# Performance work log

Hardware: AMD Instinct MI355X
Metric: run time of the kernel (lower is better)

The kernel has to match this reference:

```python
import jax, jax.numpy as jnp
import numpy as np

B, T, H, E, D, K = 4, 4096, 2048, 8, 1024, 2

def setup_inputs() -> dict:
    key = jax.random.key(0)
    ks = jax.random.split(key, 7)
    x  = jax.random.normal(ks[0], (B, T, H), dtype=jnp.float32)
    Wr = jax.random.normal(ks[1], (H, E), dtype=jnp.float32) * (1.0 / np.sqrt(H))
    br = jnp.zeros((E,), dtype=jnp.float32)
    We = jax.random.normal(ks[2], (E, H, D), dtype=jnp.float32) * (1.0 / np.sqrt(H))
    be = jnp.zeros((E, D), dtype=jnp.float32)
    Wc = jax.random.normal(ks[3], (D, H), dtype=jnp.float32) * (1.0 / np.sqrt(D))
    bc = jnp.zeros((H,), dtype=jnp.float32)
    return {"x": x, "Wr": Wr, "br": br, "We": We, "be": be, "Wc": Wc, "bc": bc}

def reference(x, Wr, br, We, be, Wc, bc):
    # Router: [B,T,H] @ [H,E] -> [B,T,E]
    router_logits = jnp.einsum('bth,he->bte', x, Wr) + br
    scores = jax.nn.softmax(router_logits, axis=-1)
    # top-k over experts (sorted descending, like torch.topk)
    topk_scores, topk_idx = jax.lax.top_k(scores, K)  # [B,T,K]
    # Dense all-expert linear: [B,T,E,D]
    expert_outs = jnp.einsum('bth,ehd->bted', x, We) + be
    # Gather the chosen experts per token: [B,T,K,D]
    gather_idx = jnp.broadcast_to(topk_idx[..., None], (B, T, K, D))
    chosen = jnp.take_along_axis(expert_outs, gather_idx, axis=2)
    # Weighted sum over top-k: [B,T,D]
    weighted = jnp.sum(chosen * topk_scores[..., None], axis=2)
    # Combine: [B,T,D] @ [D,H] -> [B,T,H]
    return jnp.einsum('btd,dh->bth', weighted, Wc) + bc
```

## Files before the change

kernel.cpp:

```cpp
#include <hip/hip_runtime.h>
#include <hip/hip_bf16.h>

typedef float f32x4 __attribute__((ext_vector_type(4)));
typedef short bf16x8 __attribute__((ext_vector_type(8)));

#define M_NT 16
#define M_OFF 17
#define M_TBL 32
#define MAX_TILES 264
#define NCHUNK 1024

__device__ __forceinline__ void gload16(const void* g, void* l) {
  __builtin_amdgcn_global_load_lds(
      (const __attribute__((address_space(1))) void*)g,
      (__attribute__((address_space(3))) void*)l, 16, 0, 0);
}

__device__ __forceinline__ float bf2f(unsigned short u) {
  union { unsigned int i; float f; } v; v.i = ((unsigned int)u) << 16; return v.f;
}
__device__ __forceinline__ unsigned short f2bf(float f) {
  __hip_bfloat16 h = __float2bfloat16(f);
  return __builtin_bit_cast(unsigned short, h);
}

#define CBAR() do { asm volatile("" ::: "memory"); __builtin_amdgcn_s_barrier(); asm volatile("" ::: "memory"); } while (0)
#define VMC4() asm volatile("s_waitcnt vmcnt(4)" ::: "memory")
#define VMC0() asm volatile("s_waitcnt vmcnt(0)" ::: "memory")

__global__ void transpose_cvt(const float* __restrict__ src,
                              unsigned short* __restrict__ dst, int R, int C) {
  __shared__ float tile[32][33];
  int b = blockIdx.z;
  int c0 = blockIdx.x * 32, r0 = blockIdx.y * 32;
  src += (size_t)b * R * C;
  dst += (size_t)b * R * C;
  int tx = threadIdx.x, ty = threadIdx.y;
#pragma unroll
  for (int i = 0; i < 32; i += 8)
    tile[ty + i][tx] = src[(size_t)(r0 + ty + i) * C + c0 + tx];
  __syncthreads();
#pragma unroll
  for (int i = 0; i < 32; i += 8)
    dst[(size_t)(c0 + ty + i) * R + r0 + tx] = f2bf(tile[tx][ty + i]);
}

__global__ __launch_bounds__(256) void router_kernel(
    const float* __restrict__ x, const float* __restrict__ Wr,
    const float* __restrict__ br, unsigned short* __restrict__ xbf,
    float* __restrict__ scores, int* __restrict__ idx,
    int* __restrict__ blk_hist) {
  __shared__ int cnt[8];
  int tid = threadIdx.x, lane = tid & 63, w = tid >> 6;
  if (tid < 8) cnt[tid] = 0;
  __syncthreads();
  int t0 = blockIdx.x * 16 + w * 4;
  const float* xr = x + (size_t)t0 * 2048;
  unsigned short* xo = xbf + (size_t)t0 * 2048;
  float acc[4][8] = {};
#pragma unroll
  for (int j = 0; j < 8; ++j) {
    int h0 = j * 256 + lane * 4;
    float4 xv[4];
#pragma unroll
    for (int t = 0; t < 4; ++t) xv[t] = *(const float4*)(xr + (size_t)t * 2048 + h0);
#pragma unroll
    for (int t = 0; t < 4; ++t) {
      ushort4 p;
      p.x = f2bf(xv[t].x); p.y = f2bf(xv[t].y);
      p.z = f2bf(xv[t].z); p.w = f2bf(xv[t].w);
      *(ushort4*)(xo + (size_t)t * 2048 + h0) = p;
    }
    const float4* wp = (const float4*)(Wr + (size_t)h0 * 8);
#pragma unroll
    for (int c = 0; c < 4; ++c) {
      float4 w0 = wp[2 * c], w1 = wp[2 * c + 1];
      float xc0 = (c == 0) ? xv[0].x : (c == 1) ? xv[0].y : (c == 2) ? xv[0].z : xv[0].w;
      float xc1 = (c == 0) ? xv[1].x : (c == 1) ? xv[1].y : (c == 2) ? xv[1].z : xv[1].w;
      float xc2 = (c == 0) ? xv[2].x : (c == 1) ? xv[2].y : (c == 2) ? xv[2].z : xv[2].w;
      float xc3 = (c == 0) ? xv[3].x : (c == 1) ? xv[3].y : (c == 2) ? xv[3].z : xv[3].w;
      acc[0][0] += xc0 * w0.x; acc[0][1] += xc0 * w0.y; acc[0][2] += xc0 * w0.z; acc[0][3] += xc0 * w0.w;
      acc[0][4] += xc0 * w1.x; acc[0][5] += xc0 * w1.y; acc[0][6] += xc0 * w1.z; acc[0][7] += xc0 * w1.w;
      acc[1][0] += xc1 * w0.x; acc[1][1] += xc1 * w0.y; acc[1][2] += xc1 * w0.z; acc[1][3] += xc1 * w0.w;
      acc[1][4] += xc1 * w1.x; acc[1][5] += xc1 * w1.y; acc[1][6] += xc1 * w1.z; acc[1][7] += xc1 * w1.w;
      acc[2][0] += xc2 * w0.x; acc[2][1] += xc2 * w0.y; acc[2][2] += xc2 * w0.z; acc[2][3] += xc2 * w0.w;
      acc[2][4] += xc2 * w1.x; acc[2][5] += xc2 * w1.y; acc[2][6] += xc2 * w1.z; acc[2][7] += xc2 * w1.w;
      acc[3][0] += xc3 * w0.x; acc[3][1] += xc3 * w0.y; acc[3][2] += xc3 * w0.z; acc[3][3] += xc3 * w0.w;
      acc[3][4] += xc3 * w1.x; acc[3][5] += xc3 * w1.y; acc[3][6] += xc3 * w1.z; acc[3][7] += xc3 * w1.w;
    }
  }
#pragma unroll
  for (int t = 0; t < 4; ++t)
#pragma unroll
    for (int e = 0; e < 8; ++e)
#pragma unroll
      for (int off = 32; off > 0; off >>= 1)
        acc[t][e] += __shfl_xor(acc[t][e], off);
  if (lane < 4) {
    int t = t0 + lane;
    float l[8];
#pragma unroll
    for (int e = 0; e < 8; ++e) {
      float v = (lane == 0) ? acc[0][e] : (lane == 1) ? acc[1][e]
              : (lane == 2) ? acc[2][e] : acc[3][e];
      l[e] = v + br[e];
    }
    float mx = l[0];
#pragma unroll
    for (int e = 1; e < 8; ++e) mx = fmaxf(mx, l[e]);
    float se = 0.f;
#pragma unroll
    for (int e = 0; e < 8; ++e) se += __expf(l[e] - mx);
    float inv = 1.f / se;
    int e1 = 0; float b1 = l[0];
#pragma unroll
    for (int e = 1; e < 8; ++e) if (l[e] > b1) { b1 = l[e]; e1 = e; }
    int e2 = -1; float b2 = -1e30f;
#pragma unroll
    for (int e = 0; e < 8; ++e) if (e != e1 && l[e] > b2) { b2 = l[e]; e2 = e; }
    idx[2 * t] = e1; idx[2 * t + 1] = e2;
    scores[2 * t] = __expf(b1 - mx) * inv;
    scores[2 * t + 1] = __expf(b2 - mx) * inv;
    atomicAdd(&cnt[e1], 1);
    atomicAdd(&cnt[e2], 1);
  }
  __syncthreads();
  if (tid < 8) blk_hist[blockIdx.x * 8 + tid] = cnt[tid];
}

__global__ __launch_bounds__(512) void scan_kernel(
    const int* __restrict__ blk_hist, int* __restrict__ chunk_base,
    int* __restrict__ meta, int* __restrict__ rowlist) {
  __shared__ int stot[8], soff[8];
  int tid = threadIdx.x, lane = tid & 63, e = tid >> 6;
  int running = 0;
  for (int g = 0; g < NCHUNK / 64; ++g) {
    int c = g * 64 + lane;
    int v = blk_hist[c * 8 + e];
    int orig = v;
#pragma unroll
    for (int off = 1; off < 64; off <<= 1) {
      int n = __shfl_up(v, off);
      if (lane >= off) v += n;
    }
    chunk_base[c * 8 + e] = running + v - orig;
    running += __shfl(v, 63);
  }
  if (lane == 0) stot[e] = running;
  __syncthreads();
  if (tid == 0) {
    int off = 0, nt = 0;
    int4* tbl = (int4*)(meta + M_TBL);
    for (int ee = 0; ee < 8; ++ee) {
      int c = stot[ee];
      meta[M_OFF + ee] = off; soff[ee] = off;
      int tiles = (c + 127) >> 7;
      for (int t = 0; t < tiles; ++t)
        tbl[nt++] = make_int4(ee, off + t * 128, min(128, c - t * 128), 0);
      off += tiles << 7;
    }
    meta[M_NT] = nt;
  }
  __syncthreads();
  for (int ee = 0; ee < 8; ++ee) {
    int c = stot[ee], end = ((c + 127) >> 7) << 7;
    for (int i = c + tid; i < end; i += 512) rowlist[soff[ee] + i] = 0;
  }
}

__global__ void scatter_kernel(const int* __restrict__ idx,
                               const int* __restrict__ chunk_base,
                               const int* __restrict__ meta,
                               int* __restrict__ rowlist) {
  int c = blockIdx.x, lane = threadIdx.x;
  int entry = c * 32 + lane;
  int e = (lane < 32) ? idx[entry] : -1;
#pragma unroll
  for (int ee = 0; ee < 8; ++ee) {
    unsigned long long m = __ballot(e == ee);
    if (e == ee) {
      int rank = __popcll(m & ((1ull << lane) - 1));
      rowlist[meta[M_OFF + ee] + chunk_base[c * 8 + ee] + rank] = entry;
    }
  }
}


#define RD_FRAGS(BUFB) do { \
  _Pragma("unroll") for (int m_ = 0; m_ < 4; ++m_) \
    av[m_] = *(const bf16x8*)(aP + (BUFB) + m_ * 1024); \
  _Pragma("unroll") for (int n_ = 0; n_ < 4; ++n_) \
    bv[n_] = *(const bf16x8*)(bP + (BUFB) + n_ * 1024); \
} while (0)

#define MFMA16() do { \
  __builtin_amdgcn_s_setprio(1); \
  _Pragma("unroll") for (int m_ = 0; m_ < 4; ++m_) \
  _Pragma("unroll") for (int n_ = 0; n_ < 4; ++n_) \
    acc[m_][n_] = __builtin_amdgcn_mfma_f32_16x16x32_bf16(av[m_], bv[n_], acc[m_][n_], 0, 0, 0); \
  __builtin_amdgcn_s_setprio(0); \
} while (0)

#define STAGE(BUFB, KOFF) do { \
  gload16(pA0 + (KOFF), dA + (BUFB)); \
  gload16(pA1 + (KOFF), dA + (BUFB) + 4096); \
  gload16(pB0 + (KOFF), dB + (BUFB)); \
  gload16(pB1 + (KOFF), dB + (BUFB) + 4096); \
} while (0)

__global__ __launch_bounds__(256, 4) void expert_gemm(
    const unsigned short* __restrict__ xbf,
    const unsigned short* __restrict__ WeT,
    const float* __restrict__ be,
    const float* __restrict__ scores,
    const int* __restrict__ rowlist,
    const int* __restrict__ meta,
    unsigned short* __restrict__ z) {
  __shared__ char smem[32768];
  __shared__ int lrows[128];
  int nt = meta[M_NT];
  int flat = blockIdx.y * 8 + blockIdx.x;
  int work = (flat & 7) * MAX_TILES + (flat >> 3);
  int tileid = work >> 3, nb = work & 7;
  if (tileid >= nt) return;
  int4 tt = ((const int4*)(meta + M_TBL))[tileid];
  int e = tt.x, base = tt.y, valid = tt.z;
  int n0 = nb * 128;
  int tid = threadIdx.x, lane = tid & 63, w = tid >> 6;
  if (tid < 128) lrows[tid] = rowlist[base + tid];
  __syncthreads();
  int wm = w >> 1, wn = w & 1;
  int fl = lane & 15, q = lane >> 4;
  int rA = tid >> 2;
  int sl = ((tid & 3) ^ ((rA >> 1) & 3)) * 16;
  const char* pA0 = (const char*)xbf + (size_t)(lrows[rA] >> 1) * 4096 + sl;
  const char* pA1 = (const char*)xbf + (size_t)(lrows[rA + 64] >> 1) * 4096 + sl;
  const char* pB0 = (const char*)WeT + ((size_t)e * 1024 + n0 + rA) * 4096 + sl;
  const char* pB1 = (const char*)WeT + ((size_t)e * 1024 + n0 + rA + 64) * 4096 + sl;
  char* dA = smem + tid * 16;
  char* dB = smem + 8192 + tid * 16;
  int swz = ((fl >> 1) & 3) << 4;
  const char* aP = smem + (wm * 64 + fl) * 64 + ((q * 16) ^ swz);
  const char* bP = smem + 8192 + (wn * 64 + fl) * 64 + ((q * 16) ^ swz);
  STAGE(0, 0); STAGE(16384, 64);
  VMC4(); CBAR();
  f32x4 acc[4][4] = {};
  bf16x8 av[4], bv[4];
  const int NT = 64;
  for (int t2 = 0; t2 < NT; t2 += 2) {
    int koff = t2 * 64;
    RD_FRAGS(0);
    MFMA16();
    CBAR();
    if (t2 + 2 < NT) { STAGE(0, koff + 128); VMC4(); } else { VMC0(); }
    CBAR();
    RD_FRAGS(16384);
    MFMA16();
    CBAR();
    if (t2 + 3 < NT) { STAGE(16384, koff + 192); VMC4(); } else { VMC0(); }
    CBAR();
  }
  float bev[4];
#pragma unroll
  for (int nc = 0; nc < 4; ++nc)
    bev[nc] = be[e * 1024 + n0 + wn * 64 + nc * 16 + fl];
#pragma unroll
  for (int mi = 0; mi < 4; ++mi) {
    int rowbase = wm * 64 + mi * 16 + q * 4;
#pragma unroll
    for (int r = 0; r < 4; ++r) {
      int row = rowbase + r;
      if (row < valid) {
        int entry = lrows[row];
        float s = scores[entry];
        unsigned short* zr = z + (size_t)entry * 1024 + n0 + wn * 64 + fl;
#pragma unroll
        for (int nc = 0; nc < 4; ++nc)
          zr[nc * 16] = f2bf((acc[mi][nc][r] + bev[nc]) * s);
      }
    }
  }
}

__global__ __launch_bounds__(256, 4) void combine_gemm(
    const unsigned short* __restrict__ y,
    const unsigned short* __restrict__ WcT,
    const float* __restrict__ bc,
    float* __restrict__ out) {
  __shared__ char smem[32768];
  int flat = blockIdx.y * 8 + blockIdx.x;
  int work = (flat & 7) * 256 + (flat >> 3);
  int mt = work >> 4, nb = work & 15;
  int m0 = mt * 128, n0 = nb * 128;
  int tid = threadIdx.x, lane = tid & 63, w = tid >> 6;
  int wm = w >> 1, wn = w & 1;
  int fl = lane & 15, q = lane >> 4;
  int rA = tid >> 2;
  int sl = ((tid & 3) ^ ((rA >> 1) & 3)) * 16;
  const char* pA0 = (const char*)y + (size_t)(m0 + rA) * 2048 + sl;
  const char* pA1 = (const char*)y + (size_t)(m0 + rA + 64) * 2048 + sl;
  const char* pB0 = (const char*)WcT + (size_t)(n0 + rA) * 2048 + sl;
  const char* pB1 = (const char*)WcT + (size_t)(n0 + rA + 64) * 2048 + sl;
  char* dA = smem + tid * 16;
  char* dB = smem + 8192 + tid * 16;
  int swz = ((fl >> 1) & 3) << 4;
  const char* aP = smem + (wm * 64 + fl) * 64 + ((q * 16) ^ swz);
  const char* bP = smem + 8192 + (wn * 64 + fl) * 64 + ((q * 16) ^ swz);
  STAGE(0, 0); STAGE(16384, 64);
  VMC4(); CBAR();
  f32x4 acc[4][4] = {};
  bf16x8 av[4], bv[4];
  const int NT = 32;
  for (int t2 = 0; t2 < NT; t2 += 2) {
    int koff = t2 * 64;
    RD_FRAGS(0);
    MFMA16();
    CBAR();
    if (t2 + 2 < NT) { STAGE(0, koff + 128); VMC4(); } else { VMC0(); }
    CBAR();
    RD_FRAGS(16384);
    MFMA16();
    CBAR();
    if (t2 + 3 < NT) { STAGE(16384, koff + 192); VMC4(); } else { VMC0(); }
    CBAR();
  }
  float bcv[4];
#pragma unroll
  for (int nc = 0; nc < 4; ++nc)
    bcv[nc] = bc[n0 + wn * 64 + nc * 16 + fl];
#pragma unroll
  for (int mi = 0; mi < 4; ++mi) {
    int rowbase = m0 + wm * 64 + mi * 16 + q * 4;
#pragma unroll
    for (int r = 0; r < 4; ++r) {
      float* orow = out + (size_t)(rowbase + r) * 2048 + n0 + wn * 64 + fl;
#pragma unroll
      for (int nc = 0; nc < 4; ++nc)
        orow[nc * 16] = acc[mi][nc][r] + bcv[nc];
    }
  }
}

__global__ void wsum_kernel(const unsigned short* __restrict__ z,
                            unsigned short* __restrict__ y) {
  size_t i = ((size_t)blockIdx.x * 256 + threadIdx.x) * 8;
  size_t t = i >> 10, d = i & 1023;
  int4 za = *(const int4*)(z + (t * 2) * 1024 + d);
  int4 zb = *(const int4*)(z + (t * 2 + 1) * 1024 + d);
  int4 r;
  const unsigned short* pa = (const unsigned short*)&za;
  const unsigned short* pb = (const unsigned short*)&zb;
  unsigned short* pr = (unsigned short*)&r;
#pragma unroll
  for (int j = 0; j < 8; ++j) pr[j] = f2bf(bf2f(pa[j]) + bf2f(pb[j]));
  *(int4*)(y + i) = r;
}

extern "C" void kernel_launch(void* const* d_in, const int* in_sizes, int n_in,
                              void* d_out, int out_size, void* d_ws, size_t ws_size,
                              hipStream_t stream) {
  const float* x  = (const float*)d_in[0];
  const float* Wr = (const float*)d_in[1];
  const float* br = (const float*)d_in[2];
  const float* We = (const float*)d_in[3];
  const float* be = (const float*)d_in[4];
  const float* Wc = (const float*)d_in[5];
  const float* bc = (const float*)d_in[6];
  float* out = (float*)d_out;

  char* ws = (char*)d_ws;
  size_t o = 0;
  auto alloc = [&](size_t b) {
    char* p = ws + o;
    o = (o + b + 255) & ~(size_t)255;
    return p;
  };
  unsigned short* xbf = (unsigned short*)alloc(16384UL * 2048 * 2);
  unsigned short* WeT = (unsigned short*)alloc(8UL * 1024 * 2048 * 2);
  unsigned short* WcT = (unsigned short*)alloc(2048UL * 1024 * 2);
  unsigned short* z   = (unsigned short*)alloc(32768UL * 1024 * 2);
  unsigned short* yw  = (unsigned short*)alloc(16384UL * 1024 * 2);
  float* scores = (float*)alloc(32768UL * 4);
  int* idx      = (int*)alloc(32768UL * 4);
  int* rowlist  = (int*)alloc(36864UL * 4);
  int* meta     = (int*)alloc(8192);
  int* blk_hist = (int*)alloc(NCHUNK * 8 * 4);
  int* chunk_base = (int*)alloc(NCHUNK * 8 * 4);
  (void)ws_size; (void)in_sizes; (void)n_in; (void)out_size;

  hipLaunchKernelGGL(transpose_cvt, dim3(32, 64, 8), dim3(32, 8), 0, stream, We, WeT, 2048, 1024);
  hipLaunchKernelGGL(transpose_cvt, dim3(64, 32, 1), dim3(32, 8), 0, stream, Wc, WcT, 1024, 2048);
  hipLaunchKernelGGL(router_kernel, dim3(NCHUNK), dim3(256), 0, stream, x, Wr, br, xbf, scores, idx, blk_hist);
  hipLaunchKernelGGL(scan_kernel, dim3(1), dim3(512), 0, stream, blk_hist, chunk_base, meta, rowlist);
  hipLaunchKernelGGL(scatter_kernel, dim3(NCHUNK), dim3(64), 0, stream, idx, chunk_base, meta, rowlist);
  hipLaunchKernelGGL(expert_gemm, dim3(8, MAX_TILES), dim3(256), 0, stream,
                     xbf, WeT, be, scores, rowlist, meta, z);
  hipLaunchKernelGGL(wsum_kernel, dim3(8192), dim3(256), 0, stream, z, yw);
  hipLaunchKernelGGL(combine_gemm, dim3(8, 256), dim3(256), 0, stream, yw, WcT, bc, out);
}
```

Baseline: 389.0 us.

## Fuse top-k weighted sum into combine GEMM A-tile loading

Removes the separate wsum kernel and its intermediate y buffer. The combine GEMM now loads the two per-token expert rows of z into registers, adds them in bf16, and writes the sum to LDS. Only the WcT tile still uses direct global-to-LDS loads. This saves a kernel launch and a write-plus-read round trip of the 32 MB y tensor. In exchange, the A operand now takes a register path with explicit lgkm waits, the A-side global reads per tile double, and launch bounds drop from 4 to 3 blocks per SM.

```diff
diff --git a/kernel.cpp b/kernel.cpp
--- a/kernel.cpp
+++ b/kernel.cpp
@@ -23,10 +23,19 @@
   __hip_bfloat16 h = __float2bfloat16(f);
   return __builtin_bit_cast(unsigned short, h);
 }
+__device__ __forceinline__ bf16x8 bfadd8(bf16x8 a, bf16x8 b) {
+  bf16x8 r;
+#pragma unroll
+  for (int j = 0; j < 8; ++j)
+    r[j] = (short)f2bf(bf2f((unsigned short)a[j]) + bf2f((unsigned short)b[j]));
+  return r;
+}
 
 #define CBAR() do { asm volatile("" ::: "memory"); __builtin_amdgcn_s_barrier(); asm volatile("" ::: "memory"); } while (0)
 #define VMC4() asm volatile("s_waitcnt vmcnt(4)" ::: "memory")
+#define VMC2() asm volatile("s_waitcnt vmcnt(2)" ::: "memory")
 #define VMC0() asm volatile("s_waitcnt vmcnt(0)" ::: "memory")
+#define LGKM0() asm volatile("s_waitcnt lgkmcnt(0)" ::: "memory")
 
 __global__ void transpose_cvt(const float* __restrict__ src,
                               unsigned short* __restrict__ dst, int R, int C) {
@@ -282,8 +291,8 @@
   }
 }
 
-__global__ __launch_bounds__(256, 4) void combine_gemm(
-    const unsigned short* __restrict__ y,
+__global__ __launch_bounds__(256, 3) void combine_gemm(
+    const unsigned short* __restrict__ z,
     const unsigned short* __restrict__ WcT,
     const float* __restrict__ bc,
     float* __restrict__ out) {
@@ -297,8 +306,10 @@
   int fl = lane & 15, q = lane >> 4;
   int rA = tid >> 2;
   int sl = ((tid & 3) ^ ((rA >> 1) & 3)) * 16;
-  const char* pA0 = (const char*)y + (size_t)(m0 + rA) * 2048 + sl;
-  const char* pA1 = (const char*)y + (size_t)(m0 + rA + 64) * 2048 + sl;
+  const char* pZa0 = (const char*)z + (size_t)(2 * (m0 + rA)) * 2048 + sl;
+  const char* pZb0 = pZa0 + 2048;
+  const char* pZa1 = (const char*)z + (size_t)(2 * (m0 + rA + 64)) * 2048 + sl;
+  const char* pZb1 = pZa1 + 2048;
   const char* pB0 = (const char*)WcT + (size_t)(n0 + rA) * 2048 + sl;
   const char* pB1 = (const char*)WcT + (size_t)(n0 + rA + 64) * 2048 + sl;
   char* dA = smem + tid * 16;
@@ -306,22 +317,69 @@
   int swz = ((fl >> 1) & 3) << 4;
   const char* aP = smem + (wm * 64 + fl) * 64 + ((q * 16) ^ swz);
   const char* bP = smem + 8192 + (wn * 64 + fl) * 64 + ((q * 16) ^ swz);
-  STAGE(0, 0); STAGE(16384, 64);
-  VMC4(); CBAR();
+  {
+    bf16x8 a0 = *(const bf16x8*)(pZa0);
+    bf16x8 b0 = *(const bf16x8*)(pZb0);
+    bf16x8 a1 = *(const bf16x8*)(pZa1);
+    bf16x8 b1 = *(const bf16x8*)(pZb1);
+    bf16x8 c0 = *(const bf16x8*)(pZa0 + 64);
+    bf16x8 d0 = *(const bf16x8*)(pZb0 + 64);
+    bf16x8 c1 = *(const bf16x8*)(pZa1 + 64);
+    bf16x8 d1 = *(const bf16x8*)(pZb1 + 64);
+    gload16(pB0, dB); gload16(pB1, dB + 4096);
+    gload16(pB0 + 64, dB + 16384); gload16(pB1 + 64, dB + 16384 + 4096);
+    *(bf16x8*)(dA) = bfadd8(a0, b0);
+    *(bf16x8*)(dA + 4096) = bfadd8(a1, b1);
+    *(bf16x8*)(dA + 16384) = bfadd8(c0, d0);
+    *(bf16x8*)(dA + 16384 + 4096) = bfadd8(c1, d1);
+  }
+  LGKM0(); VMC0(); CBAR();
   f32x4 acc[4][4] = {};
   bf16x8 av[4], bv[4];
   const int NT = 32;
   for (int t2 = 0; t2 < NT; t2 += 2) {
     int koff = t2 * 64;
+    bf16x8 za0, zb0, za1, zb1;
+    const bool pf0 = (t2 + 2) < NT;
+    if (pf0) {
+      za0 = *(const bf16x8*)(pZa0 + koff + 128);
+      zb0 = *(const bf16x8*)(pZb0 + koff + 128);
+      za1 = *(const bf16x8*)(pZa1 + koff + 128);
+      zb1 = *(const bf16x8*)(pZb1 + koff + 128);
+    }
     RD_FRAGS(0);
     MFMA16();
     CBAR();
-    if (t2 + 2 < NT) { STAGE(0, koff + 128); VMC4(); } else { VMC0(); }
-    CBAR();
+    if (pf0) {
+      gload16(pB0 + koff + 128, dB);
+      gload16(pB1 + koff + 128, dB + 4096);
+      *(bf16x8*)(dA) = bfadd8(za0, zb0);
+      *(bf16x8*)(dA + 4096) = bfadd8(za1, zb1);
+      LGKM0(); VMC2();
+    } else {
+      VMC0();
+    }
+    CBAR();
+    bf16x8 ya0, yb0, ya1, yb1;
+    const bool pf1 = (t2 + 3) < NT;
+    if (pf1) {
+      ya0 = *(const bf16x8*)(pZa0 + koff + 192);
+      yb0 = *(const bf16x8*)(pZb0 + koff + 192);
+      ya1 = *(const bf16x8*)(pZa1 + koff + 192);
+      yb1 = *(const bf16x8*)(pZb1 + koff + 192);
+    }
     RD_FRAGS(16384);
     MFMA16();
     CBAR();
-    if (t2 + 3 < NT) { STAGE(16384, koff + 192); VMC4(); } else { VMC0(); }
+    if (pf1) {
+      gload16(pB0 + koff + 192, dB + 16384);
+      gload16(pB1 + koff + 192, dB + 16384 + 4096);
+      *(bf16x8*)(dA + 16384) = bfadd8(ya0, yb0);
+      *(bf16x8*)(dA + 16384 + 4096) = bfadd8(ya1, yb1);
+      LGKM0(); VMC2();
+    } else {
+      VMC0();
+    }
     CBAR();
   }
   float bcv[4];
@@ -339,21 +397,6 @@
         orow[nc * 16] = acc[mi][nc][r] + bcv[nc];
     }
   }
-}
-
-__global__ void wsum_kernel(const unsigned short* __restrict__ z,
-                            unsigned short* __restrict__ y) {
-  size_t i = ((size_t)blockIdx.x * 256 + threadIdx.x) * 8;
-  size_t t = i >> 10, d = i & 1023;
-  int4 za = *(const int4*)(z + (t * 2) * 1024 + d);
-  int4 zb = *(const int4*)(z + (t * 2 + 1) * 1024 + d);
-  int4 r;
-  const unsigned short* pa = (const unsigned short*)&za;
-  const unsigned short* pb = (const unsigned short*)&zb;
-  unsigned short* pr = (unsigned short*)&r;
-#pragma unroll
-  for (int j = 0; j < 8; ++j) pr[j] = f2bf(bf2f(pa[j]) + bf2f(pb[j]));
-  *(int4*)(y + i) = r;
 }
 
 extern "C" void kernel_launch(void* const* d_in, const int* in_sizes, int n_in,
@@ -379,7 +422,6 @@
   unsigned short* WeT = (unsigned short*)alloc(8UL * 1024 * 2048 * 2);
   unsigned short* WcT = (unsigned short*)alloc(2048UL * 1024 * 2);
   unsigned short* z   = (unsigned short*)alloc(32768UL * 1024 * 2);
-  unsigned short* yw  = (unsigned short*)alloc(16384UL * 1024 * 2);
   float* scores = (float*)alloc(32768UL * 4);
   int* idx      = (int*)alloc(32768UL * 4);
   int* rowlist  = (int*)alloc(36864UL * 4);
@@ -395,6 +437,5 @@
   hipLaunchKernelGGL(scatter_kernel, dim3(NCHUNK), dim3(64), 0, stream, idx, chunk_base, meta, rowlist);
   hipLaunchKernelGGL(expert_gemm, dim3(8, MAX_TILES), dim3(256), 0, stream,
                      xbf, WeT, be, scores, rowlist, meta, z);
-  hipLaunchKernelGGL(wsum_kernel, dim3(8192), dim3(256), 0, stream, z, yw);
-  hipLaunchKernelGGL(combine_gemm, dim3(8, 256), dim3(256), 0, stream, yw, WcT, bc, out);
-}
+  hipLaunchKernelGGL(combine_gemm, dim3(8, 256), dim3(256), 0, stream, z, WcT, bc, out);
+}
```

Result: slower. 400.7 us (+3.0%).
